# Kernel optimization log

Measured on AMD Instinct MI355X. Metric: run time of the kernel, lower is better.

Reference implementation:

```python
import jax, jax.numpy as jnp
import numpy as np

OCC_W, SMOOTH_W, SPARSE_W, CONS_W = 1.0, 0.1, 0.01, 0.1
EPS = 1e-7  # torch BCE clamps log terms; clip preds for numerical parity


def setup_inputs() -> dict:
    key = jax.random.key(0)
    k1, k2, k3, k4 = jax.random.split(key, 4)
    N, F = 16384, 64
    predictions = jax.random.uniform(k1, (N,), dtype=jnp.float32, minval=1e-4, maxval=1.0 - 1e-4)
    targets = jax.random.uniform(k2, (N,), dtype=jnp.float32)
    features = jax.random.normal(k3, (N, F), dtype=jnp.float32)
    points = jax.random.normal(k4, (N, 3), dtype=jnp.float32)
    return {"predictions": predictions, "targets": targets, "features": features, "points": points}


def reference(predictions, targets, features, points):
    # --- occupancy loss: BCE(mean) ---
    p = jnp.clip(predictions, EPS, 1.0 - EPS)
    occupancy = -jnp.mean(targets * jnp.log(p) + (1.0 - targets) * jnp.log1p(-p))

    # --- smoothness loss: for each point, 3 nearest neighbors (excl. self) ---
    # Fused all-pairs sq-distance [N, N] + top-k, replacing the per-point python loop.
    sq = jnp.sum(points * points, axis=1)                      # [N]
    d2 = sq[:, None] + sq[None, :] - 2.0 * (points @ points.T)  # [N, N]
    d2 = jnp.maximum(d2, 0.0)  # monotone in distance, so ordering == torch.norm ordering
    _, idx = jax.lax.top_k(-d2, 4)                              # 4 smallest distances
    nn_idx = idx[:, 1:4]                                        # drop self (index 0)
    # per-point local gradient: mean |pred_i - pred_nn|, then mean over points
    smoothness = jnp.mean(jnp.abs(predictions[:, None] - predictions[nn_idx]))

    # --- sparsity loss: mean |features| ---
    sparsity = jnp.mean(jnp.abs(features))

    # --- consistency loss: MSE ---
    consistency = jnp.mean((predictions - targets) ** 2)

    total = (OCC_W * occupancy + SMOOTH_W * smoothness
             + SPARSE_W * sparsity + CONS_W * consistency)
    return total
```

## Files before the change

kernel.cpp:

```cpp
#include <hip/hip_runtime.h>
#include <float.h>
#include <math.h>


constexpr int   N_ = 16384;
constexpr int   F_ = 64;
constexpr float OCC_W = 1.0f, SMOOTH_W = 0.1f, SPARSE_W = 0.01f, CONS_W = 0.1f;
constexpr float EPS_ = 1e-7f;


__device__ __forceinline__ void ins4f(float t, float& b0, float& b1, float& b2, float& b3) {
  float n0 = fminf(b0, t);
  float n1 = __builtin_amdgcn_fmed3f(b0, b1, t);
  float n2 = __builtin_amdgcn_fmed3f(b1, b2, t);
  float n3 = __builtin_amdgcn_fmed3f(b2, b3, t);
  b0 = n0; b1 = n1; b2 = n2; b3 = n3;
}

template <int CHUNKS>
__global__ __launch_bounds__(256) void knn_kernel(const float* __restrict__ pts,
                                                  float4* __restrict__ cand,
                                                  unsigned* __restrict__ done) {
  constexpr int CHUNK   = N_ / CHUNKS;
  constexpr int TILE    = CHUNK;
  constexpr int ITEMS   = 4;
  constexpr int IPG     = 1024;
  constexpr int IGROUPS = N_ / IPG;
  if (blockIdx.x == 0 && threadIdx.x == 0) *done = 0u;

  int igrp  = blockIdx.x % IGROUPS;
  int chunk = blockIdx.x / IGROUPS;
  int j0    = chunk * CHUNK;

  __shared__ float4 tile[TILE];
  for (int t = threadIdx.x; t < TILE; t += 256) {
    int j = j0 + t;
    float x = pts[3 * j], y = pts[3 * j + 1], z = pts[3 * j + 2];
    tile[t] = make_float4(-2.f * x, -2.f * y, -2.f * z, fmaf(x, x, fmaf(y, y, z * z)));
  }

  float xi[ITEMS], yi[ITEMS], zi[ITEMS];
  float b0[ITEMS], b1[ITEMS], b2[ITEMS], b3[ITEMS];
#pragma unroll
  for (int k = 0; k < ITEMS; ++k) {
    int i = igrp * IPG + threadIdx.x + k * 256;
    xi[k] = pts[3 * i]; yi[k] = pts[3 * i + 1]; zi[k] = pts[3 * i + 2];
    b0[k] = b1[k] = b2[k] = b3[k] = FLT_MAX;
  }
  __syncthreads();

  unsigned qbase = (unsigned)(j0 >> 2);
#pragma unroll 2
  for (int jq = 0; jq < TILE; jq += 4) {
    float4 qa = tile[jq], qb = tile[jq + 1], qc = tile[jq + 2], qd = tile[jq + 3];
    unsigned qk = qbase + (unsigned)(jq >> 2);
#pragma unroll
    for (int k = 0; k < ITEMS; ++k) {
      float ta = fmaf(xi[k], qa.x, fmaf(yi[k], qa.y, fmaf(zi[k], qa.z, qa.w)));
      float tb = fmaf(xi[k], qb.x, fmaf(yi[k], qb.y, fmaf(zi[k], qb.z, qb.w)));
      float tc = fmaf(xi[k], qc.x, fmaf(yi[k], qc.y, fmaf(zi[k], qc.z, qc.w)));
      float td = fmaf(xi[k], qd.x, fmaf(yi[k], qd.y, fmaf(zi[k], qd.z, qd.w)));
      float tm = fminf(fminf(ta, tb), fminf(tc, td));
      float kf = __uint_as_float((__float_as_uint(tm) & 0xFFFFF000u) | qk);
      ins4f(kf, b0[k], b1[k], b2[k], b3[k]);
    }
  }

#pragma unroll
  for (int k = 0; k < ITEMS; ++k) {
    int i = igrp * IPG + threadIdx.x + k * 256;
    cand[(size_t)chunk * N_ + i] = make_float4(b0[k], b1[k], b2[k], b3[k]);
  }
}

template <int CHUNKS>
__global__ __launch_bounds__(256) void merge_kernel(const float* __restrict__ pred,
                                                    const float* __restrict__ targ,
                                                    const float* __restrict__ feat,
                                                    const float* __restrict__ pts,
                                                    const float4* __restrict__ cand,
                                                    float4* __restrict__ part,
                                                    unsigned* __restrict__ done,
                                                    float* __restrict__ out) {
  __shared__ float4 sh[256];
  __shared__ float ws4[4][4];
  __shared__ int is_last;
  constexpr int CPT = CHUNKS / 4;
  int tid  = threadIdx.x;
  int lane = tid & 63;
  int sub  = tid >> 6;
  int i = blockIdx.x * 64 + lane;

  const float4* f4 = (const float4*)feat;
  float s_sp = 0.f;
#pragma unroll
  for (int s = 0; s < 4; ++s) {
    float4 v = f4[(size_t)s * 65536 + blockIdx.x * 256 + tid];
    s_sp += fabsf(v.x) + fabsf(v.y) + fabsf(v.z) + fabsf(v.w);
  }

  float b0 = FLT_MAX, b1 = FLT_MAX, b2 = FLT_MAX, b3 = FLT_MAX;
#pragma unroll 4
  for (int cc = 0; cc < CPT; ++cc) {
    float4 v = cand[(size_t)(sub * CPT + cc) * N_ + i];
    ins4f(v.x, b0, b1, b2, b3);
    ins4f(v.y, b0, b1, b2, b3);
    ins4f(v.z, b0, b1, b2, b3);
    ins4f(v.w, b0, b1, b2, b3);
  }
  sh[tid] = make_float4(b0, b1, b2, b3);
  __syncthreads();

  float s_occ = 0.f, s_cons = 0.f, s_sm = 0.f;
  if (sub == 0) {
#pragma unroll
    for (int w = 1; w < 4; ++w) {
      float4 v = sh[w * 64 + lane];
      ins4f(v.x, b0, b1, b2, b3);
      ins4f(v.y, b0, b1, b2, b3);
      ins4f(v.z, b0, b1, b2, b3);
      ins4f(v.w, b0, b1, b2, b3);
    }
    unsigned qs0 = __float_as_uint(b0) & 0xFFFu;
    unsigned qs1 = __float_as_uint(b1) & 0xFFFu;
    unsigned qs2 = __float_as_uint(b2) & 0xFFFu;
    unsigned qs3 = __float_as_uint(b3) & 0xFFFu;
    float xi = pts[3 * i], yi = pts[3 * i + 1], zi = pts[3 * i + 2];
    float c0 = FLT_MAX, c1 = FLT_MAX, c2 = FLT_MAX;
    float p0 = 0.f, p1 = 0.f, p2 = 0.f;
    unsigned qarr[4] = {qs0, qs1, qs2, qs3};
#pragma unroll
    for (int s = 0; s < 4; ++s) {
#pragma unroll
      for (int m = 0; m < 4; ++m) {
        int j = (int)(qarr[s] * 4 + m);
        float dx = xi - pts[3 * j], dy = yi - pts[3 * j + 1], dz = zi - pts[3 * j + 2];
        float d2 = fmaf(dx, dx, fmaf(dy, dy, dz * dz));
        float pj = pred[j];
        if (j != i && d2 < c2) {
          bool cc0 = d2 < c0, cc1 = d2 < c1;
          float n2 = cc1 ? c1 : d2;               float m2 = cc1 ? p1 : pj;
          float n1 = cc0 ? c0 : (cc1 ? d2 : c1);  float m1 = cc0 ? p0 : (cc1 ? pj : p1);
          float n0 = cc0 ? d2 : c0;               float m0 = cc0 ? pj : p0;
          c0 = n0; c1 = n1; c2 = n2; p0 = m0; p1 = m1; p2 = m2;
        }
      }
    }
    float pi = pred[i], tg = targ[i];
    float p  = fminf(fmaxf(pi, EPS_), 1.0f - EPS_);
    s_occ  = -(tg * __logf(p) + (1.0f - tg) * __logf(1.0f - p));
    float dd = pi - tg;
    s_cons = dd * dd;
    s_sm   = fabsf(pi - p0) + fabsf(pi - p1) + fabsf(pi - p2);
  }

  for (int off = 32; off > 0; off >>= 1) {
    s_sp   += __shfl_down(s_sp, off);
    s_occ  += __shfl_down(s_occ, off);
    s_cons += __shfl_down(s_cons, off);
    s_sm   += __shfl_down(s_sm, off);
  }
  if ((tid & 63) == 0) {
    int w = tid >> 6;
    ws4[w][0] = s_occ; ws4[w][1] = s_cons; ws4[w][2] = s_sp; ws4[w][3] = s_sm;
  }
  __syncthreads();
  if (tid == 0) {
    part[blockIdx.x] = make_float4(ws4[0][0] + ws4[1][0] + ws4[2][0] + ws4[3][0],
                                   ws4[0][1] + ws4[1][1] + ws4[2][1] + ws4[3][1],
                                   ws4[0][2] + ws4[1][2] + ws4[2][2] + ws4[3][2],
                                   ws4[0][3] + ws4[1][3] + ws4[2][3] + ws4[3][3]);
    __threadfence();
    unsigned prev = atomicAdd(done, 1u);
    is_last = (prev == (unsigned)(gridDim.x - 1));
  }
  __syncthreads();

  if (is_last) {
    __threadfence();
    float4 a = part[tid];
    float o = a.x, cn = a.y, sp = a.z, sm = a.w;
    for (int off = 32; off > 0; off >>= 1) {
      o  += __shfl_down(o, off);
      cn += __shfl_down(cn, off);
      sp += __shfl_down(sp, off);
      sm += __shfl_down(sm, off);
    }
    if ((tid & 63) == 0) {
      int w = tid >> 6;
      ws4[w][0] = o; ws4[w][1] = cn; ws4[w][2] = sp; ws4[w][3] = sm;
    }
    __syncthreads();
    if (tid == 0) {
      float occ  = ws4[0][0] + ws4[1][0] + ws4[2][0] + ws4[3][0];
      float cons = ws4[0][1] + ws4[1][1] + ws4[2][1] + ws4[3][1];
      float spar = ws4[0][2] + ws4[1][2] + ws4[2][2] + ws4[3][2];
      float smoo = ws4[0][3] + ws4[1][3] + ws4[2][3] + ws4[3][3];
      out[0] = OCC_W * (occ / (float)N_)
             + CONS_W * (cons / (float)N_)
             + SPARSE_W * (spar / (float)(N_ * F_))
             + SMOOTH_W * (smoo / (float)(N_ * 3));
    }
  }
}

extern "C" void kernel_launch(void* const* d_in, const int* in_sizes, int n_in,
                              void* d_out, int out_size, void* d_ws, size_t ws_size,
                              hipStream_t stream) {
  const float* pred = (const float*)d_in[0];
  const float* targ = (const float*)d_in[1];
  const float* feat = (const float*)d_in[2];
  const float* pts  = (const float*)d_in[3];
  float* out = (float*)d_out;

  char*     ws   = (char*)d_ws;
  float4*   part = (float4*)ws;
  unsigned* done = (unsigned*)(ws + 4096);
  float4*   cand = (float4*)(ws + 8192);

  size_t base = 8192;
  auto need = [&](int c) { return base + (size_t)c * N_ * 16; };
  if (ws_size >= need(128)) {
    knn_kernel<128><<<16 * 128, 256, 0, stream>>>(pts, cand, done);
    merge_kernel<128><<<256, 256, 0, stream>>>(pred, targ, feat, pts, cand, part, done, out);
  } else if (ws_size >= need(64)) {
    knn_kernel<64><<<16 * 64, 256, 0, stream>>>(pts, cand, done);
    merge_kernel<64><<<256, 256, 0, stream>>>(pred, targ, feat, pts, cand, part, done, out);
  } else {
    knn_kernel<32><<<16 * 32, 256, 0, stream>>>(pts, cand, done);
    merge_kernel<32><<<256, 256, 0, stream>>>(pred, targ, feat, pts, cand, part, done, out);
  }
}
```

Measured before the change: 115.4 us.

## Use packed FP32 FMA over octets of candidates and coarsen KNN chunking

The distance evaluation in the KNN scan now uses v_pk_fma_f32 on pairs of candidate points. The shared tile is re-laid out as paired SoA float4s, and candidates are grouped in octets instead of quads, which halves the scalar FMA and insertion work per candidate. The merge rescans eight points per surviving octet rather than four. Chunk counts are halved (64/32/16) to fit the 12-bit octet index, which gives fewer, longer blocks and risks looser top-4 filtering, since octet minima can hide neighbors sitting in the same octet.

Result: no change. 116.8 us (+1.3%).

```diff
diff --git a/kernel.cpp b/kernel.cpp
--- a/kernel.cpp
+++ b/kernel.cpp
@@ -8,6 +8,13 @@
 constexpr float OCC_W = 1.0f, SMOOTH_W = 0.1f, SPARSE_W = 0.01f, CONS_W = 0.1f;
 constexpr float EPS_ = 1e-7f;
 
+typedef float v2f __attribute__((ext_vector_type(2)));
+
+__device__ __forceinline__ v2f pk_fma(v2f a, v2f b, v2f c) {
+  v2f d;
+  asm("v_pk_fma_f32 %0, %1, %2, %3" : "=v"(d) : "v"(a), "v"(b), "v"(c));
+  return d;
+}
 
 __device__ __forceinline__ void ins4f(float t, float& b0, float& b1, float& b2, float& b3) {
   float n0 = fminf(b0, t);
@@ -16,6 +23,7 @@
   float n3 = __builtin_amdgcn_fmed3f(b2, b3, t);
   b0 = n0; b1 = n1; b2 = n2; b3 = n3;
 }
+
 
 template <int CHUNKS>
 __global__ __launch_bounds__(256) void knn_kernel(const float* __restrict__ pts,
@@ -32,36 +40,55 @@
   int chunk = blockIdx.x / IGROUPS;
   int j0    = chunk * CHUNK;
 
-  __shared__ float4 tile[TILE];
-  for (int t = threadIdx.x; t < TILE; t += 256) {
-    int j = j0 + t;
-    float x = pts[3 * j], y = pts[3 * j + 1], z = pts[3 * j + 2];
-    tile[t] = make_float4(-2.f * x, -2.f * y, -2.f * z, fmaf(x, x, fmaf(y, y, z * z)));
-  }
-
-  float xi[ITEMS], yi[ITEMS], zi[ITEMS];
+  __shared__ float4 AB[TILE / 2];
+  __shared__ float4 CW[TILE / 2];
+  for (int p = threadIdx.x; p < TILE / 2; p += 256) {
+    int ja = j0 + 2 * p, jb = ja + 1;
+    float xa = pts[3 * ja], ya = pts[3 * ja + 1], za = pts[3 * ja + 2];
+    float xb = pts[3 * jb], yb = pts[3 * jb + 1], zb = pts[3 * jb + 2];
+    AB[p] = make_float4(-2.f * xa, -2.f * xb, -2.f * ya, -2.f * yb);
+    CW[p] = make_float4(-2.f * za, -2.f * zb,
+                        fmaf(xa, xa, fmaf(ya, ya, za * za)),
+                        fmaf(xb, xb, fmaf(yb, yb, zb * zb)));
+  }
+
+  v2f xi2[ITEMS], yi2[ITEMS], zi2[ITEMS];
   float b0[ITEMS], b1[ITEMS], b2[ITEMS], b3[ITEMS];
 #pragma unroll
   for (int k = 0; k < ITEMS; ++k) {
     int i = igrp * IPG + threadIdx.x + k * 256;
-    xi[k] = pts[3 * i]; yi[k] = pts[3 * i + 1]; zi[k] = pts[3 * i + 2];
+    float x = pts[3 * i], y = pts[3 * i + 1], z = pts[3 * i + 2];
+    xi2[k] = v2f{x, x}; yi2[k] = v2f{y, y}; zi2[k] = v2f{z, z};
     b0[k] = b1[k] = b2[k] = b3[k] = FLT_MAX;
   }
   __syncthreads();
 
-  unsigned qbase = (unsigned)(j0 >> 2);
+  unsigned obase = (unsigned)(j0 >> 3);
 #pragma unroll 2
-  for (int jq = 0; jq < TILE; jq += 4) {
-    float4 qa = tile[jq], qb = tile[jq + 1], qc = tile[jq + 2], qd = tile[jq + 3];
-    unsigned qk = qbase + (unsigned)(jq >> 2);
+  for (int oct = 0; oct < TILE / 8; ++oct) {
+    float4 ab0 = AB[oct * 4 + 0], ab1 = AB[oct * 4 + 1],
+           ab2 = AB[oct * 4 + 2], ab3 = AB[oct * 4 + 3];
+    float4 cw0 = CW[oct * 4 + 0], cw1 = CW[oct * 4 + 1],
+           cw2 = CW[oct * 4 + 2], cw3 = CW[oct * 4 + 3];
+    unsigned ok = obase + (unsigned)oct;
 #pragma unroll
     for (int k = 0; k < ITEMS; ++k) {
-      float ta = fmaf(xi[k], qa.x, fmaf(yi[k], qa.y, fmaf(zi[k], qa.z, qa.w)));
-      float tb = fmaf(xi[k], qb.x, fmaf(yi[k], qb.y, fmaf(zi[k], qb.z, qb.w)));
-      float tc = fmaf(xi[k], qc.x, fmaf(yi[k], qc.y, fmaf(zi[k], qc.z, qc.w)));
-      float td = fmaf(xi[k], qd.x, fmaf(yi[k], qd.y, fmaf(zi[k], qd.z, qd.w)));
-      float tm = fminf(fminf(ta, tb), fminf(tc, td));
-      float kf = __uint_as_float((__float_as_uint(tm) & 0xFFFFF000u) | qk);
+      v2f t0 = pk_fma(xi2[k], v2f{ab0.x, ab0.y},
+               pk_fma(yi2[k], v2f{ab0.z, ab0.w},
+               pk_fma(zi2[k], v2f{cw0.x, cw0.y}, v2f{cw0.z, cw0.w})));
+      v2f t1 = pk_fma(xi2[k], v2f{ab1.x, ab1.y},
+               pk_fma(yi2[k], v2f{ab1.z, ab1.w},
+               pk_fma(zi2[k], v2f{cw1.x, cw1.y}, v2f{cw1.z, cw1.w})));
+      v2f t2 = pk_fma(xi2[k], v2f{ab2.x, ab2.y},
+               pk_fma(yi2[k], v2f{ab2.z, ab2.w},
+               pk_fma(zi2[k], v2f{cw2.x, cw2.y}, v2f{cw2.z, cw2.w})));
+      v2f t3 = pk_fma(xi2[k], v2f{ab3.x, ab3.y},
+               pk_fma(yi2[k], v2f{ab3.z, ab3.w},
+               pk_fma(zi2[k], v2f{cw3.x, cw3.y}, v2f{cw3.z, cw3.w})));
+      float m01 = fminf(fminf(t0.x, t0.y), fminf(t1.x, t1.y));
+      float m23 = fminf(fminf(t2.x, t2.y), fminf(t3.x, t3.y));
+      float mm  = fminf(m01, m23);
+      float kf = __uint_as_float((__float_as_uint(mm) & 0xFFFFF000u) | ok);
       ins4f(kf, b0[k], b1[k], b2[k], b3[k]);
     }
   }
@@ -121,19 +148,16 @@
       ins4f(v.z, b0, b1, b2, b3);
       ins4f(v.w, b0, b1, b2, b3);
     }
-    unsigned qs0 = __float_as_uint(b0) & 0xFFFu;
-    unsigned qs1 = __float_as_uint(b1) & 0xFFFu;
-    unsigned qs2 = __float_as_uint(b2) & 0xFFFu;
-    unsigned qs3 = __float_as_uint(b3) & 0xFFFu;
+    unsigned qarr[4] = {__float_as_uint(b0) & 0xFFFu, __float_as_uint(b1) & 0xFFFu,
+                        __float_as_uint(b2) & 0xFFFu, __float_as_uint(b3) & 0xFFFu};
     float xi = pts[3 * i], yi = pts[3 * i + 1], zi = pts[3 * i + 2];
     float c0 = FLT_MAX, c1 = FLT_MAX, c2 = FLT_MAX;
     float p0 = 0.f, p1 = 0.f, p2 = 0.f;
-    unsigned qarr[4] = {qs0, qs1, qs2, qs3};
 #pragma unroll
     for (int s = 0; s < 4; ++s) {
 #pragma unroll
-      for (int m = 0; m < 4; ++m) {
-        int j = (int)(qarr[s] * 4 + m);
+      for (int m = 0; m < 8; ++m) {
+        int j = (int)(qarr[s] * 8 + m);
         float dx = xi - pts[3 * j], dy = yi - pts[3 * j + 1], dz = zi - pts[3 * j + 2];
         float d2 = fmaf(dx, dx, fmaf(dy, dy, dz * dz));
         float pj = pred[j];
@@ -220,14 +244,14 @@
 
   size_t base = 8192;
   auto need = [&](int c) { return base + (size_t)c * N_ * 16; };
-  if (ws_size >= need(128)) {
-    knn_kernel<128><<<16 * 128, 256, 0, stream>>>(pts, cand, done);
-    merge_kernel<128><<<256, 256, 0, stream>>>(pred, targ, feat, pts, cand, part, done, out);
-  } else if (ws_size >= need(64)) {
+  if (ws_size >= need(64)) {
     knn_kernel<64><<<16 * 64, 256, 0, stream>>>(pts, cand, done);
     merge_kernel<64><<<256, 256, 0, stream>>>(pred, targ, feat, pts, cand, part, done, out);
-  } else {
+  } else if (ws_size >= need(32)) {
     knn_kernel<32><<<16 * 32, 256, 0, stream>>>(pts, cand, done);
     merge_kernel<32><<<256, 256, 0, stream>>>(pred, targ, feat, pts, cand, part, done, out);
-  }
-}
+  } else {
+    knn_kernel<16><<<16 * 16, 256, 0, stream>>>(pts, cand, done);
+    merge_kernel<16><<<256, 256, 0, stream>>>(pred, targ, feat, pts, cand, part, done, out);
+  }
+}
```

## Group kNN candidates in octets with register-prefetched LDS tiles and fewer chunks

Applied to the files above, without the earlier changes.

The kNN scan now takes the running minimum over groups of eight points instead of four, tagging each group with a 12-bit octet index. This halves the number of top-4 insertions per point pair. The next octet of tile data is prefetched from LDS into registers while the current one is processed. The chunk count drops from 128 to 64, giving larger tiles, fewer blocks and a smaller candidate buffer. The merge kernel must now re-check 32 exact candidates per point instead of 16, which adds gather loads in exchange for less work in the main scan.

Measured after the change: 110.8 us (median of 2 runs). 3.9% less time.

```diff
diff --git a/kernel.cpp b/kernel.cpp
--- a/kernel.cpp
+++ b/kernel.cpp
@@ -7,7 +7,6 @@
 constexpr int   F_ = 64;
 constexpr float OCC_W = 1.0f, SMOOTH_W = 0.1f, SPARSE_W = 0.01f, CONS_W = 0.1f;
 constexpr float EPS_ = 1e-7f;
-
 
 __device__ __forceinline__ void ins4f(float t, float& b0, float& b1, float& b2, float& b3) {
   float n0 = fminf(b0, t);
@@ -17,12 +16,14 @@
   b0 = n0; b1 = n1; b2 = n2; b3 = n3;
 }
 
+
 template <int CHUNKS>
 __global__ __launch_bounds__(256) void knn_kernel(const float* __restrict__ pts,
                                                   float4* __restrict__ cand,
                                                   unsigned* __restrict__ done) {
   constexpr int CHUNK   = N_ / CHUNKS;
   constexpr int TILE    = CHUNK;
+  constexpr int NOCT    = TILE / 8;
   constexpr int ITEMS   = 4;
   constexpr int IPG     = 1024;
   constexpr int IGROUPS = N_ / IPG;
@@ -32,11 +33,11 @@
   int chunk = blockIdx.x / IGROUPS;
   int j0    = chunk * CHUNK;
 
-  __shared__ float4 tile[TILE];
+  __shared__ float4 Q[TILE];
   for (int t = threadIdx.x; t < TILE; t += 256) {
     int j = j0 + t;
     float x = pts[3 * j], y = pts[3 * j + 1], z = pts[3 * j + 2];
-    tile[t] = make_float4(-2.f * x, -2.f * y, -2.f * z, fmaf(x, x, fmaf(y, y, z * z)));
+    Q[t] = make_float4(-2.f * x, -2.f * y, -2.f * z, fmaf(x, x, fmaf(y, y, z * z)));
   }
 
   float xi[ITEMS], yi[ITEMS], zi[ITEMS];
@@ -49,21 +50,32 @@
   }
   __syncthreads();
 
-  unsigned qbase = (unsigned)(j0 >> 2);
-#pragma unroll 2
-  for (int jq = 0; jq < TILE; jq += 4) {
-    float4 qa = tile[jq], qb = tile[jq + 1], qc = tile[jq + 2], qd = tile[jq + 3];
-    unsigned qk = qbase + (unsigned)(jq >> 2);
+  unsigned obase = (unsigned)(j0 >> 3);
+
+  float4 c0 = Q[0], c1 = Q[1], c2 = Q[2], c3 = Q[3],
+         c4 = Q[4], c5 = Q[5], c6 = Q[6], c7 = Q[7];
+  for (int oct = 0; oct < NOCT; ++oct) {
+    int nb = ((oct + 1) & (NOCT - 1)) * 8;
+    float4 n0 = Q[nb + 0], n1 = Q[nb + 1], n2 = Q[nb + 2], n3 = Q[nb + 3],
+           n4 = Q[nb + 4], n5 = Q[nb + 5], n6 = Q[nb + 6], n7 = Q[nb + 7];
+    unsigned ok = obase + (unsigned)oct;
 #pragma unroll
     for (int k = 0; k < ITEMS; ++k) {
-      float ta = fmaf(xi[k], qa.x, fmaf(yi[k], qa.y, fmaf(zi[k], qa.z, qa.w)));
-      float tb = fmaf(xi[k], qb.x, fmaf(yi[k], qb.y, fmaf(zi[k], qb.z, qb.w)));
-      float tc = fmaf(xi[k], qc.x, fmaf(yi[k], qc.y, fmaf(zi[k], qc.z, qc.w)));
-      float td = fmaf(xi[k], qd.x, fmaf(yi[k], qd.y, fmaf(zi[k], qd.z, qd.w)));
-      float tm = fminf(fminf(ta, tb), fminf(tc, td));
-      float kf = __uint_as_float((__float_as_uint(tm) & 0xFFFFF000u) | qk);
+      float x = xi[k], y = yi[k], z = zi[k];
+      float t0 = fmaf(x, c0.x, fmaf(y, c0.y, fmaf(z, c0.z, c0.w)));
+      float t1 = fmaf(x, c1.x, fmaf(y, c1.y, fmaf(z, c1.z, c1.w)));
+      float t2 = fmaf(x, c2.x, fmaf(y, c2.y, fmaf(z, c2.z, c2.w)));
+      float t3 = fmaf(x, c3.x, fmaf(y, c3.y, fmaf(z, c3.z, c3.w)));
+      float t4 = fmaf(x, c4.x, fmaf(y, c4.y, fmaf(z, c4.z, c4.w)));
+      float t5 = fmaf(x, c5.x, fmaf(y, c5.y, fmaf(z, c5.z, c5.w)));
+      float t6 = fmaf(x, c6.x, fmaf(y, c6.y, fmaf(z, c6.z, c6.w)));
+      float t7 = fmaf(x, c7.x, fmaf(y, c7.y, fmaf(z, c7.z, c7.w)));
+      float m = fminf(fminf(fminf(t0, t1), fminf(t2, t3)),
+                      fminf(fminf(t4, t5), fminf(t6, t7)));
+      float kf = __uint_as_float((__float_as_uint(m) & 0xFFFFF000u) | ok);
       ins4f(kf, b0[k], b1[k], b2[k], b3[k]);
     }
+    c0 = n0; c1 = n1; c2 = n2; c3 = n3; c4 = n4; c5 = n5; c6 = n6; c7 = n7;
   }
 
 #pragma unroll
@@ -121,19 +133,16 @@
       ins4f(v.z, b0, b1, b2, b3);
       ins4f(v.w, b0, b1, b2, b3);
     }
-    unsigned qs0 = __float_as_uint(b0) & 0xFFFu;
-    unsigned qs1 = __float_as_uint(b1) & 0xFFFu;
-    unsigned qs2 = __float_as_uint(b2) & 0xFFFu;
-    unsigned qs3 = __float_as_uint(b3) & 0xFFFu;
+    unsigned qarr[4] = {__float_as_uint(b0) & 0xFFFu, __float_as_uint(b1) & 0xFFFu,
+                        __float_as_uint(b2) & 0xFFFu, __float_as_uint(b3) & 0xFFFu};
     float xi = pts[3 * i], yi = pts[3 * i + 1], zi = pts[3 * i + 2];
     float c0 = FLT_MAX, c1 = FLT_MAX, c2 = FLT_MAX;
     float p0 = 0.f, p1 = 0.f, p2 = 0.f;
-    unsigned qarr[4] = {qs0, qs1, qs2, qs3};
 #pragma unroll
     for (int s = 0; s < 4; ++s) {
 #pragma unroll
-      for (int m = 0; m < 4; ++m) {
-        int j = (int)(qarr[s] * 4 + m);
+      for (int m = 0; m < 8; ++m) {
+        int j = (int)(qarr[s] * 8 + m);
         float dx = xi - pts[3 * j], dy = yi - pts[3 * j + 1], dz = zi - pts[3 * j + 2];
         float d2 = fmaf(dx, dx, fmaf(dy, dy, dz * dz));
         float pj = pred[j];
@@ -220,14 +229,14 @@
 
   size_t base = 8192;
   auto need = [&](int c) { return base + (size_t)c * N_ * 16; };
-  if (ws_size >= need(128)) {
-    knn_kernel<128><<<16 * 128, 256, 0, stream>>>(pts, cand, done);
-    merge_kernel<128><<<256, 256, 0, stream>>>(pred, targ, feat, pts, cand, part, done, out);
-  } else if (ws_size >= need(64)) {
+  if (ws_size >= need(64)) {
     knn_kernel<64><<<16 * 64, 256, 0, stream>>>(pts, cand, done);
     merge_kernel<64><<<256, 256, 0, stream>>>(pred, targ, feat, pts, cand, part, done, out);
-  } else {
+  } else if (ws_size >= need(32)) {
     knn_kernel<32><<<16 * 32, 256, 0, stream>>>(pts, cand, done);
     merge_kernel<32><<<256, 256, 0, stream>>>(pred, targ, feat, pts, cand, part, done, out);
-  }
-}
+  } else {
+    knn_kernel<16><<<16 * 16, 256, 0, stream>>>(pts, cand, done);
+    merge_kernel<16><<<256, 256, 0, stream>>>(pred, targ, feat, pts, cand, part, done, out);
+  }
+}
```
